# Kernel optimization log

Measured on AMD Instinct MI355X. Metric: run time of the kernel, lower is better.

The kernel has to match this reference:

```python
import jax, jax.numpy as jnp
import numpy as np
from jax import lax

INPUT_DIM = 16
H1 = 5
H2 = 50
NUM_CLASSES = 20
B = 4096
T = 512


def _lstm(x, w_ih, w_hh, b_ih, b_hh, hidden):
    # x: [B, T, D]; PyTorch LSTM gate order i, f, g, o; returns all hidden states [B, T, H]
    xg = jnp.einsum('btd,gd->btg', x, w_ih) + (b_ih + b_hh)  # [B, T, 4H]
    xg_t = jnp.swapaxes(xg, 0, 1)  # [T, B, 4H]
    h0 = jnp.zeros((x.shape[0], hidden), x.dtype)
    c0 = jnp.zeros((x.shape[0], hidden), x.dtype)

    def step(carry, xt):
        h, c = carry
        g = xt + h @ w_hh.T  # [B, 4H]
        i, f, gg, o = jnp.split(g, 4, axis=-1)
        i = jax.nn.sigmoid(i)
        f = jax.nn.sigmoid(f)
        gg = jnp.tanh(gg)
        o = jax.nn.sigmoid(o)
        c = f * c + i * gg
        h = o * jnp.tanh(c)
        return (h, c), h

    _, hs = lax.scan(step, (h0, c0), xg_t)
    return jnp.swapaxes(hs, 0, 1)  # [B, T, H]


def setup_inputs() -> dict:
    key = jax.random.key(0)
    ks = jax.random.split(key, 12)
    s1 = 1.0 / np.sqrt(H1)
    s2 = 1.0 / np.sqrt(H2)
    u = lambda k, shape, s: jax.random.uniform(k, shape, jnp.float32, -s, s)
    return {
        'x': jax.random.normal(ks[0], (B, T, INPUT_DIM), jnp.float32),
        'w_ih1': u(ks[1], (4 * H1, INPUT_DIM), s1),
        'w_hh1': u(ks[2], (4 * H1, H1), s1),
        'b_ih1': u(ks[3], (4 * H1,), s1),
        'b_hh1': u(ks[4], (4 * H1,), s1),
        'w_ih2': u(ks[5], (4 * H2, H1), s2),
        'w_hh2': u(ks[6], (4 * H2, H2), s2),
        'b_ih2': u(ks[7], (4 * H2,), s2),
        'b_hh2': u(ks[8], (4 * H2,), s2),
        'fc_w': u(ks[9], (NUM_CLASSES, H2), s2),
        'fc_b': u(ks[10], (NUM_CLASSES,), s2),
    }


def reference(x, w_ih1, w_hh1, b_ih1, b_hh1, w_ih2, w_hh2, b_ih2, b_hh2, fc_w, fc_b):
    h1 = _lstm(x, w_ih1, w_hh1, b_ih1, b_hh1, H1)   # [B, T, 5]
    h2 = _lstm(h1, w_ih2, w_hh2, b_ih2, b_hh2, H2)  # [B, T, 50]
    feat = h2[:, -1, :]  # last timestep; dropout is identity in eval mode
    out = feat @ fc_w.T + fc_b  # [B, num_classes]
    return (out, feat)
```

## Files before the change

### kernel.cpp

```cpp
#include <hip/hip_runtime.h>
#include <stdint.h>

#define B_TOTAL 4096
#define T_STEPS 512
#define IN_DIM 16
#define H1 5
#define H2 50
#define NCLS 20
#define XFS 40

typedef __attribute__((ext_vector_type(8))) short bf16x8;
typedef __attribute__((ext_vector_type(4))) float f32x4;

#define LOG2E 1.44269504f
#define C2L   2.88539008f

#define CELL_UPDATE(A0_,A1_,A2_,A3_,CST_,H_) do { \
    float Ei_ = __builtin_amdgcn_exp2f(-(A0_)); \
    float Ef_ = __builtin_amdgcn_exp2f(-(A1_)); \
    float Eg_ = __builtin_amdgcn_exp2f( (A2_)); \
    float Eo_ = __builtin_amdgcn_exp2f(-(A3_)); \
    float gf_ = __builtin_amdgcn_rcpf(1.0f + Ef_); \
    float R1_ = __builtin_amdgcn_rcpf((1.0f + Ei_) * (1.0f + Eg_)); \
    float s1_ = fmaf(C2L, Eg_, -C2L); \
    CST_ = fmaf(gf_, CST_, s1_ * R1_); \
    float Ec_ = __builtin_amdgcn_exp2f(CST_); \
    float R2_ = __builtin_amdgcn_rcpf((1.0f + Eo_) * (1.0f + Ec_)); \
    H_ = (Ec_ - 1.0f) * R2_; \
  } while(0)

__device__ inline unsigned pack_top(float a, float b){
  return __builtin_amdgcn_perm(__float_as_uint(a), __float_as_uint(b), 0x07060302u);
}
__device__ inline void cvt_store(unsigned short* dh, unsigned short* dl, float4 v){
  uint2 H, L;
  H.x = pack_top(v.y, v.x);
  H.y = pack_top(v.w, v.z);
  float r0 = v.x - __uint_as_float(__float_as_uint(v.x) & 0xFFFF0000u);
  float r1 = v.y - __uint_as_float(__float_as_uint(v.y) & 0xFFFF0000u);
  float r2 = v.z - __uint_as_float(__float_as_uint(v.z) & 0xFFFF0000u);
  float r3 = v.w - __uint_as_float(__float_as_uint(v.w) & 0xFFFF0000u);
  L.x = pack_top(r1, r0);
  L.y = pack_top(r3, r2);
  *(uint2*)dh = H; *(uint2*)dl = L;
}
__device__ inline void split1(float h, unsigned short& hi, unsigned short& lo){
  unsigned u = __float_as_uint(h);
  hi = (unsigned short)(u >> 16);
  float r = h - __uint_as_float(u & 0xFFFF0000u);
  lo = (unsigned short)(__float_as_uint(r) >> 16);
}
__device__ inline void wsplit(float w, short& hi, short& lo){
  unsigned u = __float_as_uint(w);
  hi = (short)(u >> 16);
  float r = w - __uint_as_float(u & 0xFFFF0000u);
  lo = (short)(__float_as_uint(r) >> 16);
}
__device__ inline void xsplit(float4 a, float4 b, bf16x8& H, bf16x8& L){
  short h,l;
  wsplit(a.x,h,l); H[0]=h; L[0]=l;
  wsplit(a.y,h,l); H[1]=h; L[1]=l;
  wsplit(a.z,h,l); H[2]=h; L[2]=l;
  wsplit(a.w,h,l); H[3]=h; L[3]=l;
  wsplit(b.x,h,l); H[4]=h; L[4]=l;
  wsplit(b.y,h,l); H[5]=h; L[5]=l;
  wsplit(b.z,h,l); H[6]=h; L[6]=l;
  wsplit(b.w,h,l); H[7]=h; L[7]=l;
}

#define LDS_FENCE() __asm__ volatile("s_waitcnt lgkmcnt(0)" ::: "memory")
#define BARRIER()   __asm__ volatile("s_barrier" ::: "memory")

__global__ __launch_bounds__(256, 1) void lstm_fused_kernel(
    const float* __restrict__ x,
    const float* __restrict__ w_ih1, const float* __restrict__ w_hh1,
    const float* __restrict__ b_ih1, const float* __restrict__ b_hh1,
    const float* __restrict__ w_ih2, const float* __restrict__ w_hh2,
    const float* __restrict__ b_ih2, const float* __restrict__ b_hh2,
    const float* __restrict__ fc_w, const float* __restrict__ fc_b,
    float* __restrict__ out)
{
  const int tid  = threadIdx.x;
  const int lane = tid & 63;
  const int wave = tid >> 6;
  const int l15  = lane & 15;
  const int quad = lane >> 4;
  const int b0   = blockIdx.x * 16;

  __shared__ __align__(16) unsigned short a2h[2][16*72], a2l[2][16*72];
  __shared__ __align__(16) unsigned short xfh[2][16*XFS], xfl[2][16*XFS];
  __shared__ float h2f[16*52];

  const bf16x8 zero8 = {0,0,0,0,0,0,0,0};
  const f32x4  zero4 = {0.f,0.f,0.f,0.f};

  bf16x8 Bh[4][3], Bl[4][3];
  f32x4 biasv[4];
  float cst[4] = {0.f,0.f,0.f,0.f};

  const int rsw = ((l15 >> 3) & 1) << 3;
  const int wsw = (quad >> 1) << 3;

#pragma unroll
  for (int tt=0; tt<4; ++tt)
#pragma unroll
    for (int kt=0; kt<3; ++kt){ Bh[tt][kt]=zero8; Bl[tt][kt]=zero8; }

  if (wave < 3){
    const int c = wave*16 + l15;
#pragma unroll
    for (int tt=0; tt<4; ++tt){
      const float gsc = (tt == 2) ? C2L : LOG2E;
      const int grow = tt*H2 + c;
#pragma unroll
      for (int kt=0; kt<2; ++kt){
#pragma unroll
        for (int j=0;j<8;j++){
          const int kk = kt*32 + quad*8 + j;
          float w = 0.f;
          if (kk < H2)         w = w_hh2[grow*H2 + kk];
          else if (kk < H2+H1) w = w_ih2[grow*H1 + (kk-H2)];
          w *= gsc;
          short hi, lo; wsplit(w, hi, lo);
          Bh[tt][kt][j] = hi; Bl[tt][kt][j] = lo;
        }
      }
      const float bias = gsc * (b_ih2[grow] + b_hh2[grow]);
      biasv[tt][0]=bias; biasv[tt][1]=bias; biasv[tt][2]=bias; biasv[tt][3]=bias;
    }
  } else {
#pragma unroll
    for (int tt=0; tt<4; ++tt){
      const float gsc = (tt == 2) ? C2L : LOG2E;
      float bias = 0.f;
      if (l15 < 2){
        const int grow = tt*H2 + 48 + l15;
#pragma unroll
        for (int kt=0; kt<2; ++kt){
#pragma unroll
          for (int j=0;j<8;j++){
            const int kk = kt*32 + quad*8 + j;
            float w = 0.f;
            if (kk < H2)         w = w_hh2[grow*H2 + kk];
            else if (kk < H2+H1) w = w_ih2[grow*H1 + (kk-H2)];
            w *= gsc;
            short hi, lo; wsplit(w, hi, lo);
            Bh[tt][kt][j] = hi; Bl[tt][kt][j] = lo;
          }
        }
        bias = gsc * (b_ih2[grow] + b_hh2[grow]);
      } else if (l15 < 7){
        const int e = l15 - 2;
        const int grow = tt*H1 + e;
#pragma unroll
        for (int j=0;j<8;j++){
          const int kk = 32 + quad*8 + j;
          float w1 = (kk >= H2 && kk < H2+H1) ? gsc * w_hh1[grow*H1 + (kk-H2)] : 0.f;
          short hi, lo; wsplit(w1, hi, lo);
          Bh[tt][1][j] = hi; Bl[tt][1][j] = lo;
          const int k2 = quad*8 + j;
          float w2 = (k2 < IN_DIM) ? gsc * w_ih1[grow*IN_DIM + k2] : 0.f;
          wsplit(w2, hi, lo);
          Bh[tt][2][j] = hi; Bl[tt][2][j] = lo;
        }
        bias = gsc * (b_ih1[grow] + b_hh1[grow]);
      }
      biasv[tt][0]=bias; biasv[tt][1]=bias; biasv[tt][2]=bias; biasv[tt][3]=bias;
    }
  }

  { unsigned short* p = &a2h[0][0]; for (int i=tid;i<2*16*72;i+=256)  p[i]=0; }
  { unsigned short* p = &a2l[0][0]; for (int i=tid;i<2*16*72;i+=256)  p[i]=0; }
  { unsigned short* p = &xfh[0][0]; for (int i=tid;i<2*16*XFS;i+=256) p[i]=0; }
  { unsigned short* p = &xfl[0][0]; for (int i=tid;i<2*16*XFS;i+=256) p[i]=0; }
  __syncthreads();

  const bool xprod = (wave == 0);
  const int pxb = lane >> 2;
  const int pxd = (lane & 3) * 4;
  const float* pxbase = &x[(size_t)(b0+pxb)*T_STEPS*IN_DIM + pxd];
  float4 PA, PB;
  if (xprod){
    float4 v1 = *(const float4*)(pxbase + 1*IN_DIM);
    cvt_store(&xfh[1][pxb*XFS+pxd], &xfl[1][pxb*XFS+pxd], v1);
    PA = *(const float4*)(pxbase + 2*IN_DIM);
  }

  if (wave == 3){
    bf16x8 XAh = zero8, XAl = zero8;
    if (quad < 2){
      const float* xp = &x[(size_t)(b0+l15)*T_STEPS*IN_DIM + quad*8];
      xsplit(*(const float4*)xp, *(const float4*)(xp+4), XAh, XAl);
    }
    f32x4 acc[4];
#pragma unroll
    for (int tt=0; tt<4; ++tt){
      f32x4 c2 = __builtin_amdgcn_mfma_f32_16x16x32_bf16(XAh, Bh[tt][2], biasv[tt], 0,0,0);
      c2 = __builtin_amdgcn_mfma_f32_16x16x32_bf16(XAl, Bh[tt][2], c2, 0,0,0);
      c2 = __builtin_amdgcn_mfma_f32_16x16x32_bf16(XAh, Bl[tt][2], c2, 0,0,0);
      acc[tt] = c2;
    }
    const bool isl1 = (l15 >= 2) && (l15 < 7);
#pragma unroll
    for (int r=0;r<4;r++){
      float cpre = cst[r], h;
      CELL_UPDATE(acc[0][r], acc[1][r], acc[2][r], acc[3][r], cpre, h);
      if (isl1){
        cst[r] = cpre;
        unsigned short hh, hl; split1(h, hh, hl);
        const int row = quad*4 + r;
        a2h[0][row*72 + ((48 + l15) ^ wsw)] = hh;
        a2l[0][row*72 + ((48 + l15) ^ wsw)] = hl;
      }
    }
  }
  LDS_FENCE(); BARRIER();

#define MAIN_BODY(T_, RD_, WR_, PXW_, PXL_, LAST_) do { \
    if (xprod){ \
      cvt_store(&xfh[RD_][pxb*XFS+pxd], &xfl[RD_][pxb*XFS+pxd], PXW_);  \
      const int nidx_ = ((T_)+3 < T_STEPS) ? (T_)+3 : T_STEPS-1; \
      PXL_ = *(const float4*)(pxbase + (size_t)nidx_*IN_DIM);           \
    } \
    const int rb_ = l15*72; \
    bf16x8 ah0 = *(const bf16x8*)&a2h[RD_][rb_ +      ((quad*8) ^ rsw)]; \
    bf16x8 al0 = *(const bf16x8*)&a2l[RD_][rb_ +      ((quad*8) ^ rsw)]; \
    bf16x8 ah1 = *(const bf16x8*)&a2h[RD_][rb_ + 32 + ((quad*8) ^ rsw)]; \
    bf16x8 al1 = *(const bf16x8*)&a2l[RD_][rb_ + 32 + ((quad*8) ^ rsw)]; \
    f32x4 acc[4]; \
    if (wave < 3){ \
      _Pragma("unroll") \
      for (int tt=0; tt<4; ++tt){ \
        f32x4 c0 = __builtin_amdgcn_mfma_f32_16x16x32_bf16(ah0, Bh[tt][0], biasv[tt], 0,0,0); \
        c0 = __builtin_amdgcn_mfma_f32_16x16x32_bf16(al0, Bh[tt][0], c0, 0,0,0); \
        c0 = __builtin_amdgcn_mfma_f32_16x16x32_bf16(ah0, Bl[tt][0], c0, 0,0,0); \
        f32x4 c1 = __builtin_amdgcn_mfma_f32_16x16x32_bf16(ah1, Bh[tt][1], zero4, 0,0,0); \
        c1 = __builtin_amdgcn_mfma_f32_16x16x32_bf16(al1, Bh[tt][1], c1, 0,0,0); \
        c1 = __builtin_amdgcn_mfma_f32_16x16x32_bf16(ah1, Bl[tt][1], c1, 0,0,0); \
        acc[tt] = c0 + c1; \
      } \
    } else { \
      bf16x8 xfH = *(const bf16x8*)&xfh[WR_][l15*XFS + quad*8]; \
      bf16x8 xfL = *(const bf16x8*)&xfl[WR_][l15*XFS + quad*8]; \
      _Pragma("unroll") \
      for (int tt=0; tt<4; ++tt){ \
        f32x4 c0 = __builtin_amdgcn_mfma_f32_16x16x32_bf16(ah0, Bh[tt][0], biasv[tt], 0,0,0); \
        c0 = __builtin_amdgcn_mfma_f32_16x16x32_bf16(al0, Bh[tt][0], c0, 0,0,0); \
        c0 = __builtin_amdgcn_mfma_f32_16x16x32_bf16(ah0, Bl[tt][0], c0, 0,0,0); \
        f32x4 c1 = __builtin_amdgcn_mfma_f32_16x16x32_bf16(ah1, Bh[tt][1], zero4, 0,0,0); \
        c1 = __builtin_amdgcn_mfma_f32_16x16x32_bf16(al1, Bh[tt][1], c1, 0,0,0); \
        c1 = __builtin_amdgcn_mfma_f32_16x16x32_bf16(ah1, Bl[tt][1], c1, 0,0,0); \
        f32x4 c2 = __builtin_amdgcn_mfma_f32_16x16x32_bf16(xfH, Bh[tt][2], zero4, 0,0,0); \
        c2 = __builtin_amdgcn_mfma_f32_16x16x32_bf16(xfL, Bh[tt][2], c2, 0,0,0); \
        c2 = __builtin_amdgcn_mfma_f32_16x16x32_bf16(xfH, Bl[tt][2], c2, 0,0,0); \
        acc[tt] = (c0 + c1) + c2; \
      } \
    } \
     \
    if (wave < 3){ \
      const int wrb = quad*4*72 + ((wave*16 + l15) ^ wsw); \
      _Pragma("unroll") \
      for (int r=0;r<4;r++){ \
        float h; \
        CELL_UPDATE(acc[0][r], acc[1][r], acc[2][r], acc[3][r], cst[r], h); \
        unsigned short hh, hl; split1(h, hh, hl); \
        a2h[WR_][wrb + r*72] = hh; \
        a2l[WR_][wrb + r*72] = hl; \
        if (LAST_){ \
          out[(size_t)B_TOTAL*NCLS + (size_t)(b0+quad*4+r)*H2 + wave*16+l15] = h; \
          h2f[(quad*4+r)*52 + wave*16+l15] = h; \
        } \
      } \
    } else { \
      const int wrb = quad*4*72 + ((48 + l15) ^ wsw);   \
      const bool wv_ = l15 < 7; \
      _Pragma("unroll") \
      for (int r=0;r<4;r++){ \
        float h; \
        CELL_UPDATE(acc[0][r], acc[1][r], acc[2][r], acc[3][r], cst[r], h); \
        if (wv_){ \
          unsigned short hh, hl; split1(h, hh, hl); \
          a2h[WR_][wrb + r*72] = hh; \
          a2l[WR_][wrb + r*72] = hl; \
          if (LAST_ && l15 < 2){ \
            out[(size_t)B_TOTAL*NCLS + (size_t)(b0+quad*4+r)*H2 + 48+l15] = h; \
            h2f[(quad*4+r)*52 + 48+l15] = h; \
          } \
        } \
      } \
    } \
  } while(0)

  for (int t2 = 0; t2 < T_STEPS-2; t2 += 2){
    MAIN_BODY(t2,   0, 1, PA, PB, 0);
    LDS_FENCE(); BARRIER();
    MAIN_BODY(t2+1, 1, 0, PB, PA, 0);
    LDS_FENCE(); BARRIER();
  }
  MAIN_BODY(T_STEPS-2, 0, 1, PA, PB, 0);
  LDS_FENCE(); BARRIER();
  MAIN_BODY(T_STEPS-1, 1, 0, PB, PA, 1);

#undef MAIN_BODY

  __syncthreads();
  for (int i = tid; i < 16*NCLS; i += 256){
    const int b = i / NCLS, o = i % NCLS;
    float s = fc_b[o];
#pragma unroll 10
    for (int k=0;k<H2;k++) s += fc_w[o*H2+k] * h2f[b*52+k];
    out[(size_t)(b0+b)*NCLS + o] = s;
  }
}

extern "C" void kernel_launch(void* const* d_in, const int* in_sizes, int n_in,
                              void* d_out, int out_size, void* d_ws, size_t ws_size,
                              hipStream_t stream) {
  const float* x     = (const float*)d_in[0];
  const float* w_ih1 = (const float*)d_in[1];
  const float* w_hh1 = (const float*)d_in[2];
  const float* b_ih1 = (const float*)d_in[3];
  const float* b_hh1 = (const float*)d_in[4];
  const float* w_ih2 = (const float*)d_in[5];
  const float* w_hh2 = (const float*)d_in[6];
  const float* b_ih2 = (const float*)d_in[7];
  const float* b_hh2 = (const float*)d_in[8];
  const float* fc_w  = (const float*)d_in[9];
  const float* fc_b  = (const float*)d_in[10];
  float* out = (float*)d_out;

  lstm_fused_kernel<<<dim3(B_TOTAL/16), dim3(256), 0, stream>>>(
      x, w_ih1, w_hh1, b_ih1, b_hh1, w_ih2, w_hh2, b_ih2, b_hh2, fc_w, fc_b, out);
}
```

Measured before the change: 589.8 us.

## Split LSTM gate computation across two wave groups with LDS exchange

Doubles the block to 512 threads. Each tile of hidden units is now handled by two waves: the lower wave computes the i and f gates, and the upper wave computes g and o and passes them through a new shared-memory buffer. The aim is to halve the serial MFMA chain per wave on each recurrent step. The cost is one extra barrier plus an LDS round trip every timestep. The x-producer role also moves to an upper wave so its loads overlap with the cell update.

```diff
diff --git a/kernel.cpp b/kernel.cpp
--- a/kernel.cpp
+++ b/kernel.cpp
@@ -71,7 +71,7 @@
 #define LDS_FENCE() __asm__ volatile("s_waitcnt lgkmcnt(0)" ::: "memory")
 #define BARRIER()   __asm__ volatile("s_barrier" ::: "memory")
 
-__global__ __launch_bounds__(256, 1) void lstm_fused_kernel(
+__global__ __launch_bounds__(512, 1) void lstm_fused_kernel(
     const float* __restrict__ x,
     const float* __restrict__ w_ih1, const float* __restrict__ w_hh1,
     const float* __restrict__ b_ih1, const float* __restrict__ b_hh1,
@@ -83,35 +83,40 @@
   const int tid  = threadIdx.x;
   const int lane = tid & 63;
   const int wave = tid >> 6;
+  const int tile = wave & 3;
+  const bool upper = wave >= 4;
   const int l15  = lane & 15;
   const int quad = lane >> 4;
   const int b0   = blockIdx.x * 16;
 
   __shared__ __align__(16) unsigned short a2h[2][16*72], a2l[2][16*72];
   __shared__ __align__(16) unsigned short xfh[2][16*XFS], xfl[2][16*XFS];
+  __shared__ __align__(16) float pre[2][4][64][4];
   __shared__ float h2f[16*52];
 
   const bf16x8 zero8 = {0,0,0,0,0,0,0,0};
   const f32x4  zero4 = {0.f,0.f,0.f,0.f};
 
-  bf16x8 Bh[4][3], Bl[4][3];
-  f32x4 biasv[4];
+  bf16x8 Bh[2][3], Bl[2][3];
+  f32x4 biasv[2];
   float cst[4] = {0.f,0.f,0.f,0.f};
 
   const int rsw = ((l15 >> 3) & 1) << 3;
   const int wsw = (quad >> 1) << 3;
 
 #pragma unroll
-  for (int tt=0; tt<4; ++tt)
-#pragma unroll
-    for (int kt=0; kt<3; ++kt){ Bh[tt][kt]=zero8; Bl[tt][kt]=zero8; }
-
-  if (wave < 3){
-    const int c = wave*16 + l15;
-#pragma unroll
-    for (int tt=0; tt<4; ++tt){
-      const float gsc = (tt == 2) ? C2L : LOG2E;
-      const int grow = tt*H2 + c;
+  for (int t=0; t<2; ++t)
+#pragma unroll
+    for (int kt=0; kt<3; ++kt){ Bh[t][kt]=zero8; Bl[t][kt]=zero8; }
+
+#pragma unroll
+  for (int t=0; t<2; ++t){
+    const int gg = (upper ? 2 : 0) + t;
+    const float gsc = (gg == 2) ? C2L : LOG2E;
+    float bias = 0.f;
+    if (tile < 3){
+      const int c = tile*16 + l15;
+      const int grow = gg*H2 + c;
 #pragma unroll
       for (int kt=0; kt<2; ++kt){
 #pragma unroll
@@ -122,60 +127,52 @@
           else if (kk < H2+H1) w = w_ih2[grow*H1 + (kk-H2)];
           w *= gsc;
           short hi, lo; wsplit(w, hi, lo);
-          Bh[tt][kt][j] = hi; Bl[tt][kt][j] = lo;
+          Bh[t][kt][j] = hi; Bl[t][kt][j] = lo;
         }
       }
-      const float bias = gsc * (b_ih2[grow] + b_hh2[grow]);
-      biasv[tt][0]=bias; biasv[tt][1]=bias; biasv[tt][2]=bias; biasv[tt][3]=bias;
-    }
-  } else {
-#pragma unroll
-    for (int tt=0; tt<4; ++tt){
-      const float gsc = (tt == 2) ? C2L : LOG2E;
-      float bias = 0.f;
-      if (l15 < 2){
-        const int grow = tt*H2 + 48 + l15;
-#pragma unroll
-        for (int kt=0; kt<2; ++kt){
-#pragma unroll
-          for (int j=0;j<8;j++){
-            const int kk = kt*32 + quad*8 + j;
-            float w = 0.f;
-            if (kk < H2)         w = w_hh2[grow*H2 + kk];
-            else if (kk < H2+H1) w = w_ih2[grow*H1 + (kk-H2)];
-            w *= gsc;
-            short hi, lo; wsplit(w, hi, lo);
-            Bh[tt][kt][j] = hi; Bl[tt][kt][j] = lo;
-          }
+      bias = gsc * (b_ih2[grow] + b_hh2[grow]);
+    } else if (l15 < 2){
+      const int grow = gg*H2 + 48 + l15;
+#pragma unroll
+      for (int kt=0; kt<2; ++kt){
+#pragma unroll
+        for (int j=0;j<8;j++){
+          const int kk = kt*32 + quad*8 + j;
+          float w = 0.f;
+          if (kk < H2)         w = w_hh2[grow*H2 + kk];
+          else if (kk < H2+H1) w = w_ih2[grow*H1 + (kk-H2)];
+          w *= gsc;
+          short hi, lo; wsplit(w, hi, lo);
+          Bh[t][kt][j] = hi; Bl[t][kt][j] = lo;
         }
-        bias = gsc * (b_ih2[grow] + b_hh2[grow]);
-      } else if (l15 < 7){
-        const int e = l15 - 2;
-        const int grow = tt*H1 + e;
-#pragma unroll
-        for (int j=0;j<8;j++){
-          const int kk = 32 + quad*8 + j;
-          float w1 = (kk >= H2 && kk < H2+H1) ? gsc * w_hh1[grow*H1 + (kk-H2)] : 0.f;
-          short hi, lo; wsplit(w1, hi, lo);
-          Bh[tt][1][j] = hi; Bl[tt][1][j] = lo;
-          const int k2 = quad*8 + j;
-          float w2 = (k2 < IN_DIM) ? gsc * w_ih1[grow*IN_DIM + k2] : 0.f;
-          wsplit(w2, hi, lo);
-          Bh[tt][2][j] = hi; Bl[tt][2][j] = lo;
-        }
-        bias = gsc * (b_ih1[grow] + b_hh1[grow]);
       }
-      biasv[tt][0]=bias; biasv[tt][1]=bias; biasv[tt][2]=bias; biasv[tt][3]=bias;
-    }
-  }
-
-  { unsigned short* p = &a2h[0][0]; for (int i=tid;i<2*16*72;i+=256)  p[i]=0; }
-  { unsigned short* p = &a2l[0][0]; for (int i=tid;i<2*16*72;i+=256)  p[i]=0; }
-  { unsigned short* p = &xfh[0][0]; for (int i=tid;i<2*16*XFS;i+=256) p[i]=0; }
-  { unsigned short* p = &xfl[0][0]; for (int i=tid;i<2*16*XFS;i+=256) p[i]=0; }
+      bias = gsc * (b_ih2[grow] + b_hh2[grow]);
+    } else if (l15 < 7){
+      const int e = l15 - 2;
+      const int grow = gg*H1 + e;
+#pragma unroll
+      for (int j=0;j<8;j++){
+        const int kk = 32 + quad*8 + j;
+        float w1 = (kk >= H2 && kk < H2+H1) ? gsc * w_hh1[grow*H1 + (kk-H2)] : 0.f;
+        short hi, lo; wsplit(w1, hi, lo);
+        Bh[t][1][j] = hi; Bl[t][1][j] = lo;
+        const int k2 = quad*8 + j;
+        float w2 = (k2 < IN_DIM) ? gsc * w_ih1[grow*IN_DIM + k2] : 0.f;
+        wsplit(w2, hi, lo);
+        Bh[t][2][j] = hi; Bl[t][2][j] = lo;
+      }
+      bias = gsc * (b_ih1[grow] + b_hh1[grow]);
+    }
+    biasv[t][0]=bias; biasv[t][1]=bias; biasv[t][2]=bias; biasv[t][3]=bias;
+  }
+
+  { unsigned short* p = &a2h[0][0]; for (int i=tid;i<2*16*72;i+=512)  p[i]=0; }
+  { unsigned short* p = &a2l[0][0]; for (int i=tid;i<2*16*72;i+=512)  p[i]=0; }
+  { unsigned short* p = &xfh[0][0]; for (int i=tid;i<2*16*XFS;i+=512) p[i]=0; }
+  { unsigned short* p = &xfl[0][0]; for (int i=tid;i<2*16*XFS;i+=512) p[i]=0; }
   __syncthreads();
 
-  const bool xprod = (wave == 0);
+  const bool xprod = (wave == 4);
   const int pxb = lane >> 2;
   const int pxd = (lane & 3) * 4;
   const float* pxbase = &x[(size_t)(b0+pxb)*T_STEPS*IN_DIM + pxd];
@@ -186,25 +183,34 @@
     PA = *(const float4*)(pxbase + 2*IN_DIM);
   }
 
-  if (wave == 3){
+  f32x4 pacc0 = zero4, pacc1 = zero4;
+  if (tile == 3){
     bf16x8 XAh = zero8, XAl = zero8;
     if (quad < 2){
       const float* xp = &x[(size_t)(b0+l15)*T_STEPS*IN_DIM + quad*8];
       xsplit(*(const float4*)xp, *(const float4*)(xp+4), XAh, XAl);
     }
-    f32x4 acc[4];
-#pragma unroll
-    for (int tt=0; tt<4; ++tt){
-      f32x4 c2 = __builtin_amdgcn_mfma_f32_16x16x32_bf16(XAh, Bh[tt][2], biasv[tt], 0,0,0);
-      c2 = __builtin_amdgcn_mfma_f32_16x16x32_bf16(XAl, Bh[tt][2], c2, 0,0,0);
-      c2 = __builtin_amdgcn_mfma_f32_16x16x32_bf16(XAh, Bl[tt][2], c2, 0,0,0);
-      acc[tt] = c2;
-    }
+#pragma unroll
+    for (int t=0; t<2; ++t){
+      f32x4 c2 = __builtin_amdgcn_mfma_f32_16x16x32_bf16(XAh, Bh[t][2], biasv[t], 0,0,0);
+      c2 = __builtin_amdgcn_mfma_f32_16x16x32_bf16(XAl, Bh[t][2], c2, 0,0,0);
+      c2 = __builtin_amdgcn_mfma_f32_16x16x32_bf16(XAh, Bl[t][2], c2, 0,0,0);
+      if (t == 0) pacc0 = c2; else pacc1 = c2;
+    }
+    if (upper){
+      *(f32x4*)&pre[0][3][lane][0] = pacc0;
+      *(f32x4*)&pre[1][3][lane][0] = pacc1;
+    }
+  }
+  LDS_FENCE(); BARRIER();
+  if (tile == 3 && !upper){
+    f32x4 g4 = *(const f32x4*)&pre[0][3][lane][0];
+    f32x4 o4 = *(const f32x4*)&pre[1][3][lane][0];
     const bool isl1 = (l15 >= 2) && (l15 < 7);
 #pragma unroll
     for (int r=0;r<4;r++){
       float cpre = cst[r], h;
-      CELL_UPDATE(acc[0][r], acc[1][r], acc[2][r], acc[3][r], cpre, h);
+      CELL_UPDATE(pacc0[r], pacc1[r], g4[r], o4[r], cpre, h);
       if (isl1){
         cst[r] = cpre;
         unsigned short hh, hl; split1(h, hh, hl);
@@ -217,94 +223,95 @@
   LDS_FENCE(); BARRIER();
 
 #define MAIN_BODY(T_, RD_, WR_, PXW_, PXL_, LAST_) do { \
-    if (xprod){ \
-      cvt_store(&xfh[RD_][pxb*XFS+pxd], &xfl[RD_][pxb*XFS+pxd], PXW_);  \
-      const int nidx_ = ((T_)+3 < T_STEPS) ? (T_)+3 : T_STEPS-1; \
-      PXL_ = *(const float4*)(pxbase + (size_t)nidx_*IN_DIM);           \
-    } \
+     \
     const int rb_ = l15*72; \
     bf16x8 ah0 = *(const bf16x8*)&a2h[RD_][rb_ +      ((quad*8) ^ rsw)]; \
     bf16x8 al0 = *(const bf16x8*)&a2l[RD_][rb_ +      ((quad*8) ^ rsw)]; \
     bf16x8 ah1 = *(const bf16x8*)&a2h[RD_][rb_ + 32 + ((quad*8) ^ rsw)]; \
     bf16x8 al1 = *(const bf16x8*)&a2l[RD_][rb_ + 32 + ((quad*8) ^ rsw)]; \
-    f32x4 acc[4]; \
-    if (wave < 3){ \
-      _Pragma("unroll") \
-      for (int tt=0; tt<4; ++tt){ \
-        f32x4 c0 = __builtin_amdgcn_mfma_f32_16x16x32_bf16(ah0, Bh[tt][0], biasv[tt], 0,0,0); \
-        c0 = __builtin_amdgcn_mfma_f32_16x16x32_bf16(al0, Bh[tt][0], c0, 0,0,0); \
-        c0 = __builtin_amdgcn_mfma_f32_16x16x32_bf16(ah0, Bl[tt][0], c0, 0,0,0); \
-        f32x4 c1 = __builtin_amdgcn_mfma_f32_16x16x32_bf16(ah1, Bh[tt][1], zero4, 0,0,0); \
-        c1 = __builtin_amdgcn_mfma_f32_16x16x32_bf16(al1, Bh[tt][1], c1, 0,0,0); \
-        c1 = __builtin_amdgcn_mfma_f32_16x16x32_bf16(ah1, Bl[tt][1], c1, 0,0,0); \
-        acc[tt] = c0 + c1; \
-      } \
-    } else { \
-      bf16x8 xfH = *(const bf16x8*)&xfh[WR_][l15*XFS + quad*8]; \
-      bf16x8 xfL = *(const bf16x8*)&xfl[WR_][l15*XFS + quad*8]; \
-      _Pragma("unroll") \
-      for (int tt=0; tt<4; ++tt){ \
-        f32x4 c0 = __builtin_amdgcn_mfma_f32_16x16x32_bf16(ah0, Bh[tt][0], biasv[tt], 0,0,0); \
-        c0 = __builtin_amdgcn_mfma_f32_16x16x32_bf16(al0, Bh[tt][0], c0, 0,0,0); \
-        c0 = __builtin_amdgcn_mfma_f32_16x16x32_bf16(ah0, Bl[tt][0], c0, 0,0,0); \
-        f32x4 c1 = __builtin_amdgcn_mfma_f32_16x16x32_bf16(ah1, Bh[tt][1], zero4, 0,0,0); \
-        c1 = __builtin_amdgcn_mfma_f32_16x16x32_bf16(al1, Bh[tt][1], c1, 0,0,0); \
-        c1 = __builtin_amdgcn_mfma_f32_16x16x32_bf16(ah1, Bl[tt][1], c1, 0,0,0); \
-        f32x4 c2 = __builtin_amdgcn_mfma_f32_16x16x32_bf16(xfH, Bh[tt][2], zero4, 0,0,0); \
-        c2 = __builtin_amdgcn_mfma_f32_16x16x32_bf16(xfL, Bh[tt][2], c2, 0,0,0); \
-        c2 = __builtin_amdgcn_mfma_f32_16x16x32_bf16(xfH, Bl[tt][2], c2, 0,0,0); \
-        acc[tt] = (c0 + c1) + c2; \
-      } \
+    bf16x8 xH = zero8, xL = zero8; \
+    if (tile == 3){ \
+      xH = *(const bf16x8*)&xfh[WR_][l15*XFS + quad*8]; \
+      xL = *(const bf16x8*)&xfl[WR_][l15*XFS + quad*8]; \
     } \
+    f32x4 acc0, acc1; \
+    _Pragma("unroll") \
+    for (int t=0; t<2; ++t){ \
+      f32x4 c0 = __builtin_amdgcn_mfma_f32_16x16x32_bf16(ah0, Bh[t][0], biasv[t], 0,0,0); \
+      c0 = __builtin_amdgcn_mfma_f32_16x16x32_bf16(al0, Bh[t][0], c0, 0,0,0); \
+      c0 = __builtin_amdgcn_mfma_f32_16x16x32_bf16(ah0, Bl[t][0], c0, 0,0,0); \
+      f32x4 c1 = __builtin_amdgcn_mfma_f32_16x16x32_bf16(ah1, Bh[t][1], zero4, 0,0,0); \
+      c1 = __builtin_amdgcn_mfma_f32_16x16x32_bf16(al1, Bh[t][1], c1, 0,0,0); \
+      c1 = __builtin_amdgcn_mfma_f32_16x16x32_bf16(ah1, Bl[t][1], c1, 0,0,0); \
+      f32x4 s_; \
+      if (tile == 3){ \
+        f32x4 c2 = __builtin_amdgcn_mfma_f32_16x16x32_bf16(xH, Bh[t][2], zero4, 0,0,0); \
+        c2 = __builtin_amdgcn_mfma_f32_16x16x32_bf16(xL, Bh[t][2], c2, 0,0,0); \
+        c2 = __builtin_amdgcn_mfma_f32_16x16x32_bf16(xH, Bl[t][2], c2, 0,0,0); \
+        s_ = (c0 + c1) + c2; \
+      } else s_ = c0 + c1; \
+      if (t == 0) acc0 = s_; else acc1 = s_; \
+    } \
+    if (upper){ \
+      *(f32x4*)&pre[0][tile][lane][0] = acc0; \
+      *(f32x4*)&pre[1][tile][lane][0] = acc1; \
+    } \
+    LDS_FENCE(); BARRIER();    \
      \
-    if (wave < 3){ \
-      const int wrb = quad*4*72 + ((wave*16 + l15) ^ wsw); \
-      _Pragma("unroll") \
-      for (int r=0;r<4;r++){ \
-        float h; \
-        CELL_UPDATE(acc[0][r], acc[1][r], acc[2][r], acc[3][r], cst[r], h); \
-        unsigned short hh, hl; split1(h, hh, hl); \
-        a2h[WR_][wrb + r*72] = hh; \
-        a2l[WR_][wrb + r*72] = hl; \
-        if (LAST_){ \
-          out[(size_t)B_TOTAL*NCLS + (size_t)(b0+quad*4+r)*H2 + wave*16+l15] = h; \
-          h2f[(quad*4+r)*52 + wave*16+l15] = h; \
-        } \
-      } \
-    } else { \
-      const int wrb = quad*4*72 + ((48 + l15) ^ wsw);   \
-      const bool wv_ = l15 < 7; \
-      _Pragma("unroll") \
-      for (int r=0;r<4;r++){ \
-        float h; \
-        CELL_UPDATE(acc[0][r], acc[1][r], acc[2][r], acc[3][r], cst[r], h); \
-        if (wv_){ \
+    if (!upper){ \
+      f32x4 g4 = *(const f32x4*)&pre[0][tile][lane][0]; \
+      f32x4 o4 = *(const f32x4*)&pre[1][tile][lane][0]; \
+      if (tile < 3){ \
+        const int wrb = quad*4*72 + ((tile*16 + l15) ^ wsw); \
+        _Pragma("unroll") \
+        for (int r=0;r<4;r++){ \
+          float h; \
+          CELL_UPDATE(acc0[r], acc1[r], g4[r], o4[r], cst[r], h); \
           unsigned short hh, hl; split1(h, hh, hl); \
           a2h[WR_][wrb + r*72] = hh; \
           a2l[WR_][wrb + r*72] = hl; \
-          if (LAST_ && l15 < 2){ \
-            out[(size_t)B_TOTAL*NCLS + (size_t)(b0+quad*4+r)*H2 + 48+l15] = h; \
-            h2f[(quad*4+r)*52 + 48+l15] = h; \
+          if (LAST_){ \
+            out[(size_t)B_TOTAL*NCLS + (size_t)(b0+quad*4+r)*H2 + tile*16+l15] = h; \
+            h2f[(quad*4+r)*52 + tile*16+l15] = h; \
+          } \
+        } \
+      } else { \
+        const int wrb = quad*4*72 + ((48 + l15) ^ wsw); \
+        const bool wv_ = l15 < 7; \
+        _Pragma("unroll") \
+        for (int r=0;r<4;r++){ \
+          float h; \
+          CELL_UPDATE(acc0[r], acc1[r], g4[r], o4[r], cst[r], h); \
+          if (wv_){ \
+            unsigned short hh, hl; split1(h, hh, hl); \
+            a2h[WR_][wrb + r*72] = hh; \
+            a2l[WR_][wrb + r*72] = hl; \
+            if (LAST_ && l15 < 2){ \
+              out[(size_t)B_TOTAL*NCLS + (size_t)(b0+quad*4+r)*H2 + 48+l15] = h; \
+              h2f[(quad*4+r)*52 + 48+l15] = h; \
+            } \
           } \
         } \
       } \
+    } else if (xprod){ \
+      cvt_store(&xfh[RD_][pxb*XFS+pxd], &xfl[RD_][pxb*XFS+pxd], PXW_);  \
+      const int nidx_ = ((T_)+3 < T_STEPS) ? (T_)+3 : T_STEPS-1; \
+      PXL_ = *(const float4*)(pxbase + (size_t)nidx_*IN_DIM);           \
     } \
+    LDS_FENCE(); BARRIER();    \
   } while(0)
 
   for (int t2 = 0; t2 < T_STEPS-2; t2 += 2){
     MAIN_BODY(t2,   0, 1, PA, PB, 0);
-    LDS_FENCE(); BARRIER();
     MAIN_BODY(t2+1, 1, 0, PB, PA, 0);
-    LDS_FENCE(); BARRIER();
   }
   MAIN_BODY(T_STEPS-2, 0, 1, PA, PB, 0);
-  LDS_FENCE(); BARRIER();
   MAIN_BODY(T_STEPS-1, 1, 0, PB, PA, 1);
 
 #undef MAIN_BODY
 
   __syncthreads();
-  for (int i = tid; i < 16*NCLS; i += 256){
+  for (int i = tid; i < 16*NCLS; i += 512){
     const int b = i / NCLS, o = i % NCLS;
     float s = fc_b[o];
 #pragma unroll 10
@@ -329,6 +336,6 @@
   const float* fc_b  = (const float*)d_in[10];
   float* out = (float*)d_out;
 
-  lstm_fused_kernel<<<dim3(B_TOTAL/16), dim3(256), 0, stream>>>(
+  lstm_fused_kernel<<<dim3(B_TOTAL/16), dim3(512), 0, stream>>>(
       x, w_ih1, w_hh1, b_ih1, b_hh1, w_ih2, w_hh2, b_ih2, b_hh2, fc_w, fc_b, out);
 }
```

Measured after the change: 629.6 us. +6.7%, slower.
